# Performance work log

Measured on AMD Instinct MI355X. Metric: run time of the kernel, lower is better.

Reference implementation:

```python
import jax, jax.numpy as jnp
import numpy as np

B, S, D, H, N, K, Ks = 2, 1024, 1024, 1024, 8, 2, 1


def setup_inputs() -> dict:
    key = jax.random.key(0)
    k0, k1, k2, k3 = jax.random.split(key, 4)
    x_BSD = jax.random.normal(k0, (B, S, D), dtype=jnp.float32)
    Wg_DN = jax.random.normal(k1, (D, N), dtype=jnp.float32) * (D ** -0.5)
    Wl1_ND2H = jax.random.normal(k2, (N, D, 2 * H), dtype=jnp.float32) * 0.02
    Wl2_NHD = jax.random.normal(k3, (N, H, D), dtype=jnp.float32) * 0.02
    # aux-loss-free routing biases: 0 for routed experts, -inf for shared slots
    biases_N = jnp.concatenate([
        jnp.zeros((N - Ks,), dtype=jnp.float32),
        jnp.full((Ks,), -jnp.inf, dtype=jnp.float32),
    ])
    return {"x_BSD": x_BSD, "Wg_DN": Wg_DN, "Wl1_ND2H": Wl1_ND2H,
            "Wl2_NHD": Wl2_NHD, "biases_N": biases_N}


def reference(x_BSD, Wg_DN, Wl1_ND2H, Wl2_NHD, biases_N):
    Bb, Ss, Dd = x_BSD.shape
    Nn = Wg_DN.shape[1]
    x_MD = x_BSD.reshape(-1, Dd)                      # [M, D]

    # ---- TopKRouter: sigmoid scores, bias-adjusted top-k selection ----
    logits_MN = x_MD @ Wg_DN                          # [M, N]
    scores_MN = jax.nn.sigmoid(logits_MN)
    kr = K - Ks                                       # routed experts per token
    _, idx_Mk = jax.lax.top_k(scores_MN + biases_N, kr)
    w_Mk = jnp.take_along_axis(scores_MN, idx_Mk, axis=1)
    w_Mk = w_Mk / (jnp.sum(w_Mk, axis=-1, keepdims=True) + 1e-9)  # normalize gates
    oh_MkN = jax.nn.one_hot(idx_Mk, Nn, dtype=x_MD.dtype)
    s_MN = jnp.einsum('mkn,mk->mn', oh_MkN, w_Mk)     # routed gate weights
    mask_MN = jnp.sum(oh_MkN, axis=1)
    # shared experts (last Ks slots): always active with weight 1
    shared_N = (jnp.arange(Nn) >= Nn - Ks)
    s_MN = jnp.where(shared_N, 1.0, s_MN)
    mask_MN = jnp.where(shared_N, 1.0, mask_MN)
    w_NM = (s_MN * mask_MN).T                         # [N, M] combine weights

    # ---- MoMoE: SwiGLU experts, dense compute with zero weight for unrouted ----
    gu_NM2H = jnp.einsum('md,ndh->nmh', x_MD, Wl1_ND2H)   # [N, M, 2H]
    g_NMH, u_NMH = jnp.split(gu_NM2H, 2, axis=-1)
    h_NMH = jax.nn.silu(g_NMH) * u_NMH
    y_MD = jnp.einsum('nmh,nhd,nm->md', h_NMH, Wl2_NHD, w_NM)
    return y_MD.reshape(Bb, Ss, Dd)
```

## Files before the change

kernel.cpp:

```cpp
#include <hip/hip_runtime.h>
#include <hip/hip_bf16.h>
#include <math.h>

#define M_TOK 2048
#define D_DIM 1024
#define H_DIM 1024
#define N_EXP 8
#define N_ROUTED 7
#define MAXT 40

typedef __hip_bfloat16 bf16;
typedef float f32x4 __attribute__((ext_vector_type(4)));
typedef short bf16x8 __attribute__((ext_vector_type(8)));

#define GLOAD16(gp, lp)                                                     \
  __builtin_amdgcn_global_load_lds(                                         \
      (const __attribute__((address_space(1))) void*)(gp),                  \
      (__attribute__((address_space(3))) void*)(lp), 16, 0, 0)

__global__ __launch_bounds__(256)
void routing_kernel(const float* __restrict__ x,
                    const float* __restrict__ Wg,
                    float* __restrict__ w_out,
                    int* __restrict__ cnt,
                    int* __restrict__ perm) {
  const int lane = threadIdx.x & 63;
  const int m = blockIdx.x * 4 + (threadIdx.x >> 6);
  if (m >= M_TOK) return;
  float acc[N_EXP];
#pragma unroll
  for (int n = 0; n < N_EXP; ++n) acc[n] = 0.f;
  const float* xr = x + (size_t)m * D_DIM;
  for (int d = lane; d < D_DIM; d += 64) {
    const float xv = xr[d];
    const float4 wa = *reinterpret_cast<const float4*>(Wg + (size_t)d * N_EXP);
    const float4 wb = *reinterpret_cast<const float4*>(Wg + (size_t)d * N_EXP + 4);
    acc[0] = fmaf(xv, wa.x, acc[0]);
    acc[1] = fmaf(xv, wa.y, acc[1]);
    acc[2] = fmaf(xv, wa.z, acc[2]);
    acc[3] = fmaf(xv, wa.w, acc[3]);
    acc[4] = fmaf(xv, wb.x, acc[4]);
    acc[5] = fmaf(xv, wb.y, acc[5]);
    acc[6] = fmaf(xv, wb.z, acc[6]);
    acc[7] = fmaf(xv, wb.w, acc[7]);
  }
#pragma unroll
  for (int n = 0; n < N_EXP; ++n) {
#pragma unroll
    for (int off = 32; off > 0; off >>= 1)
      acc[n] += __shfl_xor(acc[n], off, 64);
  }
  if (lane == 0) {
    int bi = 0;
    float bl = acc[0];
#pragma unroll
    for (int n = 1; n < N_ROUTED; ++n) {
      if (acc[n] > bl) { bl = acc[n]; bi = n; }
    }
    const float s = 1.f / (1.f + expf(-bl));
    w_out[m] = s / (s + 1e-9f);
    const int pos = atomicAdd(&cnt[bi], 1);
    perm[bi * M_TOK + pos] = m;
  }
}

__global__ void tilemap_kernel(const int* __restrict__ cnt,
                               int* __restrict__ tmap, int* __restrict__ ntiles) {
  if (threadIdx.x == 0 && blockIdx.x == 0) {
    int t = 0;
    for (int n = 0; n < N_ROUTED; ++n) {
      const int c = cnt[n];
      for (int r = 0; r < c; r += 128) { tmap[2 * t] = n; tmap[2 * t + 1] = r; ++t; }
    }
    for (int r = 0; r < M_TOK; r += 128) { tmap[2 * t] = N_EXP - 1; tmap[2 * t + 1] = r; ++t; }
    ntiles[0] = t;
    for (int u = t; u < MAXT; ++u) { tmap[2 * u] = 0; tmap[2 * u + 1] = 0; }
  }
}

__global__ __launch_bounds__(256)
void convx_kernel(const float* __restrict__ in, bf16* __restrict__ outb) {
  const int i = blockIdx.x * 256 + threadIdx.x;
  const float4 a = reinterpret_cast<const float4*>(in)[i * 2];
  const float4 b = reinterpret_cast<const float4*>(in)[i * 2 + 1];
  union { bf16 h[8]; uint4 q; } u;
  u.h[0] = __float2bfloat16(a.x); u.h[1] = __float2bfloat16(a.y);
  u.h[2] = __float2bfloat16(a.z); u.h[3] = __float2bfloat16(a.w);
  u.h[4] = __float2bfloat16(b.x); u.h[5] = __float2bfloat16(b.y);
  u.h[6] = __float2bfloat16(b.z); u.h[7] = __float2bfloat16(b.w);
  reinterpret_cast<uint4*>(outb)[i] = u.q;
}

__global__ __launch_bounds__(256)
void transconv_kernel(const float* __restrict__ in, bf16* __restrict__ outb,
                      int R, int C) {
  __shared__ float tile[64][65];
  const int t = threadIdx.x;
  const float* inp = in + (size_t)blockIdx.z * R * C;
  bf16* outp = outb + (size_t)blockIdx.z * R * C;
  const int c0 = blockIdx.x * 64, r0 = blockIdx.y * 64;
  const int lr = t >> 4, lc4 = (t & 15) * 4;
#pragma unroll
  for (int rep = 0; rep < 4; ++rep) {
    const float4 v = *reinterpret_cast<const float4*>(
        inp + (size_t)(r0 + lr + rep * 16) * C + c0 + lc4);
    float* dst = &tile[lr + rep * 16][lc4];
    dst[0] = v.x; dst[1] = v.y; dst[2] = v.z; dst[3] = v.w;
  }
  __syncthreads();
  const int seg = t & 7;
#pragma unroll
  for (int rep = 0; rep < 2; ++rep) {
    const int oc = (t >> 3) + rep * 32;
    union { bf16 h[8]; uint4 q; } u;
#pragma unroll
    for (int j = 0; j < 8; ++j) u.h[j] = __float2bfloat16(tile[seg * 8 + j][oc]);
    *reinterpret_cast<uint4*>(outp + (size_t)(c0 + oc) * R + r0 + seg * 8) = u.q;
  }
}

__global__ __launch_bounds__(256, 2)
void l1_kernel(const bf16* __restrict__ xb,
               const bf16* __restrict__ W1t,
               const int* __restrict__ perm,
               const int* __restrict__ cnt,
               const int* __restrict__ tmap,
               const int* __restrict__ ntiles,
               bf16* __restrict__ hbuf) {
  const int ti = blockIdx.y;
  if (ti >= ntiles[0]) return;
  const int n = tmap[2 * ti], row0 = tmap[2 * ti + 1];
  const int nt = blockIdx.x;
  const int c = (n == N_EXP - 1) ? M_TOK : cnt[n];

  __shared__ bf16 L0[16384];
  __shared__ bf16 L1[16384];

  const int t = threadIdx.x;
  const int trow = t >> 3;
  const int gk = ((t & 7) ^ (trow & 7)) * 8;

  int tokr[4];
#pragma unroll
  for (int p = 0; p < 4; ++p) {
    const int lr = row0 + p * 32 + trow;
    tokr[p] = (n == N_EXP - 1) ? lr : perm[n * M_TOK + (lr < c ? lr : row0)];
  }
  const bf16* gA0 = xb + (size_t)tokr[0] * D_DIM + gk;
  const bf16* gA1 = xb + (size_t)tokr[1] * D_DIM + gk;
  const bf16* gA2 = xb + (size_t)tokr[2] * D_DIM + gk;
  const bf16* gA3 = xb + (size_t)tokr[3] * D_DIM + gk;
  const bf16* gBg0 = W1t + ((size_t)n * 2048 + nt * 64 + trow) * D_DIM + gk;
  const bf16* gBg1 = gBg0 + (size_t)32 * D_DIM;
  const bf16* gBu0 = gBg0 + (size_t)H_DIM * D_DIM;
  const bf16* gBu1 = gBg1 + (size_t)H_DIM * D_DIM;

#define L1_STAGE(BUF, KT) do {                                   \
    const int ko = (KT) * 64;                                    \
    GLOAD16(gA0 + ko, &BUF[(0 * 256 + t) * 8]);                  \
    GLOAD16(gA1 + ko, &BUF[(1 * 256 + t) * 8]);                  \
    GLOAD16(gA2 + ko, &BUF[(2 * 256 + t) * 8]);                  \
    GLOAD16(gA3 + ko, &BUF[(3 * 256 + t) * 8]);                  \
    GLOAD16(gBg0 + ko, &BUF[8192 + (0 * 256 + t) * 8]);          \
    GLOAD16(gBg1 + ko, &BUF[8192 + (1 * 256 + t) * 8]);          \
    GLOAD16(gBu0 + ko, &BUF[12288 + (0 * 256 + t) * 8]);         \
    GLOAD16(gBu1 + ko, &BUF[12288 + (1 * 256 + t) * 8]);         \
  } while (0)

  const int lane = t & 63, wid = t >> 6;
  const int wm = wid >> 1, wn = wid & 1;
  const int l15 = lane & 15, lhi = lane >> 4, l7 = l15 & 7;

  f32x4 accg[4][2], accu[4][2];
#pragma unroll
  for (int i = 0; i < 4; ++i)
#pragma unroll
    for (int j = 0; j < 2; ++j) {
      accg[i][j] = (f32x4){0.f, 0.f, 0.f, 0.f};
      accu[i][j] = (f32x4){0.f, 0.f, 0.f, 0.f};
    }

#define L1_COMPUTE(BUF) do {                                                   \
    bf16x8 a[4][2], bg[2][2], bu[2][2];                                        \
    _Pragma("unroll") for (int kk = 0; kk < 2; ++kk) {                         \
      const int sl = ((kk * 4 + lhi) ^ l7) * 8;                                \
      _Pragma("unroll") for (int fm = 0; fm < 4; ++fm)                         \
        a[fm][kk] = *reinterpret_cast<const bf16x8*>(                          \
            &BUF[(wm * 64 + fm * 16 + l15) * 64 + sl]);                        \
      _Pragma("unroll") for (int fn = 0; fn < 2; ++fn) {                       \
        bg[fn][kk] = *reinterpret_cast<const bf16x8*>(                         \
            &BUF[8192 + (wn * 32 + fn * 16 + l15) * 64 + sl]);                 \
        bu[fn][kk] = *reinterpret_cast<const bf16x8*>(                         \
            &BUF[12288 + (wn * 32 + fn * 16 + l15) * 64 + sl]);                \
      }                                                                        \
    }                                                                          \
    _Pragma("unroll") for (int kk = 0; kk < 2; ++kk)                           \
    _Pragma("unroll") for (int fm = 0; fm < 4; ++fm)                           \
    _Pragma("unroll") for (int fn = 0; fn < 2; ++fn) {                         \
      accg[fm][fn] = __builtin_amdgcn_mfma_f32_16x16x32_bf16(                  \
          a[fm][kk], bg[fn][kk], accg[fm][fn], 0, 0, 0);                       \
      accu[fm][fn] = __builtin_amdgcn_mfma_f32_16x16x32_bf16(                  \
          a[fm][kk], bu[fn][kk], accu[fm][fn], 0, 0, 0);                       \
    }                                                                          \
  } while (0)

  L1_STAGE(L0, 0);
  __syncthreads();
  for (int it = 0; it < 8; ++it) {
    L1_STAGE(L1, 2 * it + 1);
    L1_COMPUTE(L0);
    __syncthreads();
    if (it < 7) L1_STAGE(L0, 2 * it + 2);
    L1_COMPUTE(L1);
    __syncthreads();
  }

  bf16* hp = hbuf + (size_t)n * M_TOK * H_DIM;
#pragma unroll
  for (int fm = 0; fm < 4; ++fm)
#pragma unroll
    for (int fn = 0; fn < 2; ++fn)
#pragma unroll
      for (int r = 0; r < 4; ++r) {
        const int mrow = row0 + wm * 64 + fm * 16 + lhi * 4 + r;
        const int col = nt * 64 + wn * 32 + fn * 16 + l15;
        const float g = accg[fm][fn][r];
        const float u = accu[fm][fn][r];
        const float h = g * u / (1.f + __expf(-g));
        hp[(size_t)mrow * H_DIM + col] = __float2bfloat16(h);
      }
#undef L1_STAGE
#undef L1_COMPUTE
}

__global__ __launch_bounds__(256, 4)
void l2_kernel(const bf16* __restrict__ hbuf,
               const bf16* __restrict__ W2t,
               const int* __restrict__ perm,
               const int* __restrict__ cnt,
               const int* __restrict__ tmap,
               const int* __restrict__ ntiles,
               const float* __restrict__ wtok,
               float* __restrict__ out) {
  const int ti = blockIdx.y;
  if (ti >= ntiles[0]) return;
  const int n = tmap[2 * ti], row0 = tmap[2 * ti + 1];
  const int nt = blockIdx.x;
  const int c = (n == N_EXP - 1) ? M_TOK : cnt[n];

  __shared__ bf16 L0[12288];
  __shared__ bf16 L1[12288];

  const int t = threadIdx.x;
  const int trow = t >> 3;
  const int gk = ((t & 7) ^ (trow & 7)) * 8;

  const bf16* hp = hbuf + (size_t)n * M_TOK * H_DIM;
  const bf16* gA0 = hp + (size_t)(row0 + trow) * H_DIM + gk;
  const bf16* gA1 = gA0 + (size_t)32 * H_DIM;
  const bf16* gA2 = gA0 + (size_t)64 * H_DIM;
  const bf16* gA3 = gA0 + (size_t)96 * H_DIM;
  const bf16* gB0 = W2t + ((size_t)n * D_DIM + nt * 64 + trow) * H_DIM + gk;
  const bf16* gB1 = gB0 + (size_t)32 * H_DIM;

#define L2_STAGE(BUF, KT) do {                                   \
    const int ko = (KT) * 64;                                    \
    GLOAD16(gA0 + ko, &BUF[(0 * 256 + t) * 8]);                  \
    GLOAD16(gA1 + ko, &BUF[(1 * 256 + t) * 8]);                  \
    GLOAD16(gA2 + ko, &BUF[(2 * 256 + t) * 8]);                  \
    GLOAD16(gA3 + ko, &BUF[(3 * 256 + t) * 8]);                  \
    GLOAD16(gB0 + ko, &BUF[8192 + (0 * 256 + t) * 8]);           \
    GLOAD16(gB1 + ko, &BUF[8192 + (1 * 256 + t) * 8]);           \
  } while (0)

  const int lane = t & 63, wid = t >> 6;
  const int wm = wid >> 1, wn = wid & 1;
  const int l15 = lane & 15, lhi = lane >> 4, l7 = l15 & 7;

  f32x4 acc[4][2];
#pragma unroll
  for (int i = 0; i < 4; ++i)
#pragma unroll
    for (int j = 0; j < 2; ++j) acc[i][j] = (f32x4){0.f, 0.f, 0.f, 0.f};

#define L2_COMPUTE(BUF) do {                                                   \
    bf16x8 a[4][2], b[2][2];                                                   \
    _Pragma("unroll") for (int kk = 0; kk < 2; ++kk) {                         \
      const int sl = ((kk * 4 + lhi) ^ l7) * 8;                                \
      _Pragma("unroll") for (int fm = 0; fm < 4; ++fm)                         \
        a[fm][kk] = *reinterpret_cast<const bf16x8*>(                          \
            &BUF[(wm * 64 + fm * 16 + l15) * 64 + sl]);                        \
      _Pragma("unroll") for (int fn = 0; fn < 2; ++fn)                         \
        b[fn][kk] = *reinterpret_cast<const bf16x8*>(                          \
            &BUF[8192 + (wn * 32 + fn * 16 + l15) * 64 + sl]);                 \
    }                                                                          \
    _Pragma("unroll") for (int kk = 0; kk < 2; ++kk)                           \
    _Pragma("unroll") for (int fm = 0; fm < 4; ++fm)                           \
    _Pragma("unroll") for (int fn = 0; fn < 2; ++fn)                           \
      acc[fm][fn] = __builtin_amdgcn_mfma_f32_16x16x32_bf16(                   \
          a[fm][kk], b[fn][kk], acc[fm][fn], 0, 0, 0);                         \
  } while (0)

  L2_STAGE(L0, 0);
  __syncthreads();
  for (int it = 0; it < 8; ++it) {
    L2_STAGE(L1, 2 * it + 1);
    L2_COMPUTE(L0);
    __syncthreads();
    if (it < 7) L2_STAGE(L0, 2 * it + 2);
    L2_COMPUTE(L1);
    __syncthreads();
  }

#pragma unroll
  for (int fm = 0; fm < 4; ++fm)
#pragma unroll
    for (int r = 0; r < 4; ++r) {
      const int mrow = row0 + wm * 64 + fm * 16 + lhi * 4 + r;
      if (mrow < row0 + 128 && mrow - row0 + (row0) < c + 0 ? (mrow < c) : false) {}
      if (mrow < c) {
        const int tok = (n == N_EXP - 1) ? mrow : perm[n * M_TOK + mrow];
        const float wt = (n == N_EXP - 1) ? 1.f : wtok[tok];
        const size_t base = (size_t)tok * D_DIM + nt * 64 + wn * 32 + l15;
        atomicAdd(&out[base], wt * acc[fm][0][r]);
        atomicAdd(&out[base + 16], wt * acc[fm][1][r]);
      }
    }
#undef L2_STAGE
#undef L2_COMPUTE
}

extern "C" void kernel_launch(void* const* d_in, const int* in_sizes, int n_in,
                              void* d_out, int out_size, void* d_ws, size_t ws_size,
                              hipStream_t stream) {
  const float* x   = (const float*)d_in[0];
  const float* Wg  = (const float*)d_in[1];
  const float* Wl1 = (const float*)d_in[2];
  const float* Wl2 = (const float*)d_in[3];
  float* out = (float*)d_out;

  char* ws = (char*)d_ws;
  int*   cnt    = (int*)(ws + 0);
  float* wtok   = (float*)(ws + 1024);
  int*   perm   = (int*)(ws + 16384);
  int*   tmap   = (int*)(ws + 81920);
  int*   ntiles = (int*)(ws + 83968);
  bf16*  xb   = (bf16*)(ws + (1ull << 20));
  bf16*  W1t  = (bf16*)(ws + (8ull << 20));
  bf16*  W2t  = (bf16*)(ws + (40ull << 20));
  bf16*  hbuf = (bf16*)(ws + (56ull << 20));

  hipMemsetAsync(cnt, 0, N_EXP * sizeof(int), stream);
  hipMemsetAsync(out, 0, (size_t)M_TOK * D_DIM * sizeof(float), stream);

  convx_kernel<<<M_TOK * D_DIM / 8 / 256, 256, 0, stream>>>(x, xb);
  transconv_kernel<<<dim3(2 * H_DIM / 64, D_DIM / 64, N_EXP), 256, 0, stream>>>(
      Wl1, W1t, D_DIM, 2 * H_DIM);
  transconv_kernel<<<dim3(D_DIM / 64, H_DIM / 64, N_EXP), 256, 0, stream>>>(
      Wl2, W2t, H_DIM, D_DIM);
  routing_kernel<<<M_TOK / 4, 256, 0, stream>>>(x, Wg, wtok, cnt, perm);
  tilemap_kernel<<<1, 64, 0, stream>>>(cnt, tmap, ntiles);

  l1_kernel<<<dim3(16, MAXT), 256, 0, stream>>>(xb, W1t, perm, cnt, tmap, ntiles, hbuf);
  l2_kernel<<<dim3(16, MAXT), 256, 0, stream>>>(hbuf, W2t, perm, cnt, tmap, ntiles, wtok, out);
}
```

Before: 246.8 us.

## Halve GEMM N-tile to double grid size and fuse x conversion into routing

```diff
diff --git a/kernel.cpp b/kernel.cpp
--- a/kernel.cpp
+++ b/kernel.cpp
@@ -21,6 +21,7 @@
 __global__ __launch_bounds__(256)
 void routing_kernel(const float* __restrict__ x,
                     const float* __restrict__ Wg,
+                    bf16* __restrict__ xb,
                     float* __restrict__ w_out,
                     int* __restrict__ cnt,
                     int* __restrict__ perm) {
@@ -31,8 +32,10 @@
 #pragma unroll
   for (int n = 0; n < N_EXP; ++n) acc[n] = 0.f;
   const float* xr = x + (size_t)m * D_DIM;
+  bf16* xbr = xb + (size_t)m * D_DIM;
   for (int d = lane; d < D_DIM; d += 64) {
     const float xv = xr[d];
+    xbr[d] = __float2bfloat16(xv);
     const float4 wa = *reinterpret_cast<const float4*>(Wg + (size_t)d * N_EXP);
     const float4 wb = *reinterpret_cast<const float4*>(Wg + (size_t)d * N_EXP + 4);
     acc[0] = fmaf(xv, wa.x, acc[0]);
@@ -79,19 +82,6 @@
 }
 
 __global__ __launch_bounds__(256)
-void convx_kernel(const float* __restrict__ in, bf16* __restrict__ outb) {
-  const int i = blockIdx.x * 256 + threadIdx.x;
-  const float4 a = reinterpret_cast<const float4*>(in)[i * 2];
-  const float4 b = reinterpret_cast<const float4*>(in)[i * 2 + 1];
-  union { bf16 h[8]; uint4 q; } u;
-  u.h[0] = __float2bfloat16(a.x); u.h[1] = __float2bfloat16(a.y);
-  u.h[2] = __float2bfloat16(a.z); u.h[3] = __float2bfloat16(a.w);
-  u.h[4] = __float2bfloat16(b.x); u.h[5] = __float2bfloat16(b.y);
-  u.h[6] = __float2bfloat16(b.z); u.h[7] = __float2bfloat16(b.w);
-  reinterpret_cast<uint4*>(outb)[i] = u.q;
-}
-
-__global__ __launch_bounds__(256)
 void transconv_kernel(const float* __restrict__ in, bf16* __restrict__ outb,
                       int R, int C) {
   __shared__ float tile[64][65];
@@ -119,7 +109,7 @@
   }
 }
 
-__global__ __launch_bounds__(256, 2)
+__global__ __launch_bounds__(256, 3)
 void l1_kernel(const bf16* __restrict__ xb,
                const bf16* __restrict__ W1t,
                const int* __restrict__ perm,
@@ -133,8 +123,8 @@
   const int nt = blockIdx.x;
   const int c = (n == N_EXP - 1) ? M_TOK : cnt[n];
 
-  __shared__ bf16 L0[16384];
-  __shared__ bf16 L1[16384];
+  __shared__ bf16 L0[12288];
+  __shared__ bf16 L1[12288];
 
   const int t = threadIdx.x;
   const int trow = t >> 3;
@@ -150,10 +140,8 @@
   const bf16* gA1 = xb + (size_t)tokr[1] * D_DIM + gk;
   const bf16* gA2 = xb + (size_t)tokr[2] * D_DIM + gk;
   const bf16* gA3 = xb + (size_t)tokr[3] * D_DIM + gk;
-  const bf16* gBg0 = W1t + ((size_t)n * 2048 + nt * 64 + trow) * D_DIM + gk;
-  const bf16* gBg1 = gBg0 + (size_t)32 * D_DIM;
-  const bf16* gBu0 = gBg0 + (size_t)H_DIM * D_DIM;
-  const bf16* gBu1 = gBg1 + (size_t)H_DIM * D_DIM;
+  const bf16* gBg = W1t + ((size_t)n * 2048 + nt * 32 + trow) * D_DIM + gk;
+  const bf16* gBu = gBg + (size_t)H_DIM * D_DIM;
 
 #define L1_STAGE(BUF, KT) do {                                   \
     const int ko = (KT) * 64;                                    \
@@ -161,46 +149,39 @@
     GLOAD16(gA1 + ko, &BUF[(1 * 256 + t) * 8]);                  \
     GLOAD16(gA2 + ko, &BUF[(2 * 256 + t) * 8]);                  \
     GLOAD16(gA3 + ko, &BUF[(3 * 256 + t) * 8]);                  \
-    GLOAD16(gBg0 + ko, &BUF[8192 + (0 * 256 + t) * 8]);          \
-    GLOAD16(gBg1 + ko, &BUF[8192 + (1 * 256 + t) * 8]);          \
-    GLOAD16(gBu0 + ko, &BUF[12288 + (0 * 256 + t) * 8]);         \
-    GLOAD16(gBu1 + ko, &BUF[12288 + (1 * 256 + t) * 8]);         \
+    GLOAD16(gBg + ko, &BUF[8192 + t * 8]);                       \
+    GLOAD16(gBu + ko, &BUF[10240 + t * 8]);                      \
   } while (0)
 
   const int lane = t & 63, wid = t >> 6;
   const int wm = wid >> 1, wn = wid & 1;
   const int l15 = lane & 15, lhi = lane >> 4, l7 = l15 & 7;
 
-  f32x4 accg[4][2], accu[4][2];
-#pragma unroll
-  for (int i = 0; i < 4; ++i)
-#pragma unroll
-    for (int j = 0; j < 2; ++j) {
-      accg[i][j] = (f32x4){0.f, 0.f, 0.f, 0.f};
-      accu[i][j] = (f32x4){0.f, 0.f, 0.f, 0.f};
-    }
+  f32x4 accg[4], accu[4];
+#pragma unroll
+  for (int i = 0; i < 4; ++i) {
+    accg[i] = (f32x4){0.f, 0.f, 0.f, 0.f};
+    accu[i] = (f32x4){0.f, 0.f, 0.f, 0.f};
+  }
 
 #define L1_COMPUTE(BUF) do {                                                   \
-    bf16x8 a[4][2], bg[2][2], bu[2][2];                                        \
+    bf16x8 a[4][2], bg[2], bu[2];                                              \
     _Pragma("unroll") for (int kk = 0; kk < 2; ++kk) {                         \
       const int sl = ((kk * 4 + lhi) ^ l7) * 8;                                \
       _Pragma("unroll") for (int fm = 0; fm < 4; ++fm)                         \
         a[fm][kk] = *reinterpret_cast<const bf16x8*>(                          \
             &BUF[(wm * 64 + fm * 16 + l15) * 64 + sl]);                        \
-      _Pragma("unroll") for (int fn = 0; fn < 2; ++fn) {                       \
-        bg[fn][kk] = *reinterpret_cast<const bf16x8*>(                         \
-            &BUF[8192 + (wn * 32 + fn * 16 + l15) * 64 + sl]);                 \
-        bu[fn][kk] = *reinterpret_cast<const bf16x8*>(                         \
-            &BUF[12288 + (wn * 32 + fn * 16 + l15) * 64 + sl]);                \
-      }                                                                        \
+      bg[kk] = *reinterpret_cast<const bf16x8*>(                               \
+          &BUF[8192 + (wn * 16 + l15) * 64 + sl]);                             \
+      bu[kk] = *reinterpret_cast<const bf16x8*>(                               \
+          &BUF[10240 + (wn * 16 + l15) * 64 + sl]);                            \
     }                                                                          \
     _Pragma("unroll") for (int kk = 0; kk < 2; ++kk)                           \
-    _Pragma("unroll") for (int fm = 0; fm < 4; ++fm)                           \
-    _Pragma("unroll") for (int fn = 0; fn < 2; ++fn) {                         \
-      accg[fm][fn] = __builtin_amdgcn_mfma_f32_16x16x32_bf16(                  \
-          a[fm][kk], bg[fn][kk], accg[fm][fn], 0, 0, 0);                       \
-      accu[fm][fn] = __builtin_amdgcn_mfma_f32_16x16x32_bf16(                  \
-          a[fm][kk], bu[fn][kk], accu[fm][fn], 0, 0, 0);                       \
+    _Pragma("unroll") for (int fm = 0; fm < 4; ++fm) {                         \
+      accg[fm] = __builtin_amdgcn_mfma_f32_16x16x32_bf16(                      \
+          a[fm][kk], bg[kk], accg[fm], 0, 0, 0);                               \
+      accu[fm] = __builtin_amdgcn_mfma_f32_16x16x32_bf16(                      \
+          a[fm][kk], bu[kk], accu[fm], 0, 0, 0);                               \
     }                                                                          \
   } while (0)
 
@@ -216,24 +197,22 @@
   }
 
   bf16* hp = hbuf + (size_t)n * M_TOK * H_DIM;
+  const int col = nt * 32 + wn * 16 + l15;
 #pragma unroll
   for (int fm = 0; fm < 4; ++fm)
 #pragma unroll
-    for (int fn = 0; fn < 2; ++fn)
-#pragma unroll
-      for (int r = 0; r < 4; ++r) {
-        const int mrow = row0 + wm * 64 + fm * 16 + lhi * 4 + r;
-        const int col = nt * 64 + wn * 32 + fn * 16 + l15;
-        const float g = accg[fm][fn][r];
-        const float u = accu[fm][fn][r];
-        const float h = g * u / (1.f + __expf(-g));
-        hp[(size_t)mrow * H_DIM + col] = __float2bfloat16(h);
-      }
+    for (int r = 0; r < 4; ++r) {
+      const int mrow = row0 + wm * 64 + fm * 16 + lhi * 4 + r;
+      const float g = accg[fm][r];
+      const float u = accu[fm][r];
+      const float h = g * u / (1.f + __expf(-g));
+      hp[(size_t)mrow * H_DIM + col] = __float2bfloat16(h);
+    }
 #undef L1_STAGE
 #undef L1_COMPUTE
 }
 
-__global__ __launch_bounds__(256, 4)
+__global__ __launch_bounds__(256, 3)
 void l2_kernel(const bf16* __restrict__ hbuf,
                const bf16* __restrict__ W2t,
                const int* __restrict__ perm,
@@ -248,8 +227,8 @@
   const int nt = blockIdx.x;
   const int c = (n == N_EXP - 1) ? M_TOK : cnt[n];
 
-  __shared__ bf16 L0[12288];
-  __shared__ bf16 L1[12288];
+  __shared__ bf16 L0[10240];
+  __shared__ bf16 L1[10240];
 
   const int t = threadIdx.x;
   const int trow = t >> 3;
@@ -260,8 +239,7 @@
   const bf16* gA1 = gA0 + (size_t)32 * H_DIM;
   const bf16* gA2 = gA0 + (size_t)64 * H_DIM;
   const bf16* gA3 = gA0 + (size_t)96 * H_DIM;
-  const bf16* gB0 = W2t + ((size_t)n * D_DIM + nt * 64 + trow) * H_DIM + gk;
-  const bf16* gB1 = gB0 + (size_t)32 * H_DIM;
+  const bf16* gB = W2t + ((size_t)n * D_DIM + nt * 32 + trow) * H_DIM + gk;
 
 #define L2_STAGE(BUF, KT) do {                                   \
     const int ko = (KT) * 64;                                    \
@@ -269,36 +247,31 @@
     GLOAD16(gA1 + ko, &BUF[(1 * 256 + t) * 8]);                  \
     GLOAD16(gA2 + ko, &BUF[(2 * 256 + t) * 8]);                  \
     GLOAD16(gA3 + ko, &BUF[(3 * 256 + t) * 8]);                  \
-    GLOAD16(gB0 + ko, &BUF[8192 + (0 * 256 + t) * 8]);           \
-    GLOAD16(gB1 + ko, &BUF[8192 + (1 * 256 + t) * 8]);           \
+    GLOAD16(gB + ko, &BUF[8192 + t * 8]);                        \
   } while (0)
 
   const int lane = t & 63, wid = t >> 6;
   const int wm = wid >> 1, wn = wid & 1;
   const int l15 = lane & 15, lhi = lane >> 4, l7 = l15 & 7;
 
-  f32x4 acc[4][2];
-#pragma unroll
-  for (int i = 0; i < 4; ++i)
-#pragma unroll
-    for (int j = 0; j < 2; ++j) acc[i][j] = (f32x4){0.f, 0.f, 0.f, 0.f};
+  f32x4 acc[4];
+#pragma unroll
+  for (int i = 0; i < 4; ++i) acc[i] = (f32x4){0.f, 0.f, 0.f, 0.f};
 
 #define L2_COMPUTE(BUF) do {                                                   \
-    bf16x8 a[4][2], b[2][2];                                                   \
+    bf16x8 a[4][2], b[2];                                                      \
     _Pragma("unroll") for (int kk = 0; kk < 2; ++kk) {                         \
       const int sl = ((kk * 4 + lhi) ^ l7) * 8;                                \
       _Pragma("unroll") for (int fm = 0; fm < 4; ++fm)                         \
         a[fm][kk] = *reinterpret_cast<const bf16x8*>(                          \
             &BUF[(wm * 64 + fm * 16 + l15) * 64 + sl]);                        \
-      _Pragma("unroll") for (int fn = 0; fn < 2; ++fn)                         \
-        b[fn][kk] = *reinterpret_cast<const bf16x8*>(                          \
-            &BUF[8192 + (wn * 32 + fn * 16 + l15) * 64 + sl]);                 \
+      b[kk] = *reinterpret_cast<const bf16x8*>(                                \
+          &BUF[8192 + (wn * 16 + l15) * 64 + sl]);                             \
     }                                                                          \
     _Pragma("unroll") for (int kk = 0; kk < 2; ++kk)                           \
     _Pragma("unroll") for (int fm = 0; fm < 4; ++fm)                           \
-    _Pragma("unroll") for (int fn = 0; fn < 2; ++fn)                           \
-      acc[fm][fn] = __builtin_amdgcn_mfma_f32_16x16x32_bf16(                   \
-          a[fm][kk], b[fn][kk], acc[fm][fn], 0, 0, 0);                         \
+      acc[fm] = __builtin_amdgcn_mfma_f32_16x16x32_bf16(                       \
+          a[fm][kk], b[kk], acc[fm], 0, 0, 0);                                 \
   } while (0)
 
   L2_STAGE(L0, 0);
@@ -312,18 +285,16 @@
     __syncthreads();
   }
 
+  const int colb = nt * 32 + wn * 16 + l15;
 #pragma unroll
   for (int fm = 0; fm < 4; ++fm)
 #pragma unroll
     for (int r = 0; r < 4; ++r) {
       const int mrow = row0 + wm * 64 + fm * 16 + lhi * 4 + r;
-      if (mrow < row0 + 128 && mrow - row0 + (row0) < c + 0 ? (mrow < c) : false) {}
       if (mrow < c) {
         const int tok = (n == N_EXP - 1) ? mrow : perm[n * M_TOK + mrow];
         const float wt = (n == N_EXP - 1) ? 1.f : wtok[tok];
-        const size_t base = (size_t)tok * D_DIM + nt * 64 + wn * 32 + l15;
-        atomicAdd(&out[base], wt * acc[fm][0][r]);
-        atomicAdd(&out[base + 16], wt * acc[fm][1][r]);
+        atomicAdd(&out[(size_t)tok * D_DIM + colb], wt * acc[fm][r]);
       }
     }
 #undef L2_STAGE
@@ -353,14 +324,13 @@
   hipMemsetAsync(cnt, 0, N_EXP * sizeof(int), stream);
   hipMemsetAsync(out, 0, (size_t)M_TOK * D_DIM * sizeof(float), stream);
 
-  convx_kernel<<<M_TOK * D_DIM / 8 / 256, 256, 0, stream>>>(x, xb);
   transconv_kernel<<<dim3(2 * H_DIM / 64, D_DIM / 64, N_EXP), 256, 0, stream>>>(
       Wl1, W1t, D_DIM, 2 * H_DIM);
   transconv_kernel<<<dim3(D_DIM / 64, H_DIM / 64, N_EXP), 256, 0, stream>>>(
       Wl2, W2t, H_DIM, D_DIM);
-  routing_kernel<<<M_TOK / 4, 256, 0, stream>>>(x, Wg, wtok, cnt, perm);
+  routing_kernel<<<M_TOK / 4, 256, 0, stream>>>(x, Wg, xb, wtok, cnt, perm);
   tilemap_kernel<<<1, 64, 0, stream>>>(cnt, tmap, ntiles);
 
-  l1_kernel<<<dim3(16, MAXT), 256, 0, stream>>>(xb, W1t, perm, cnt, tmap, ntiles, hbuf);
-  l2_kernel<<<dim3(16, MAXT), 256, 0, stream>>>(hbuf, W2t, perm, cnt, tmap, ntiles, wtok, out);
-}
+  l1_kernel<<<dim3(32, MAXT), 256, 0, stream>>>(xb, W1t, perm, cnt, tmap, ntiles, hbuf);
+  l2_kernel<<<dim3(32, MAXT), 256, 0, stream>>>(hbuf, W2t, perm, cnt, tmap, ntiles, wtok, out);
+}
```

Result: no change. 245.6 us (-0.5%).
